# Kernel tuning notes

Hardware: AMD Instinct MI355X
Metric: run time of the kernel (lower is better)

## Reference

```python
import jax, jax.numpy as jnp
import numpy as np

K = 5          # top_k periods
KERNEL = 25    # moving-average kernel for series decomposition
D = 64         # d_model / channels
EPS = 1e-5     # BatchNorm eps (torch default)


def setup_inputs() -> dict:
    key = jax.random.key(0)
    k0, k1, k2, k3, k4 = jax.random.split(key, 5)
    B, T = 8, 2048
    x = jax.random.normal(k0, (B, T, D), jnp.float32)
    w1 = jax.random.normal(k1, (D, D, 3, 3), jnp.float32) * 0.05
    w2 = jax.random.normal(k2, (D, D, 3, 3), jnp.float32) * 0.05
    bn1_gamma = jnp.ones((D,), jnp.float32) + 0.1 * jax.random.normal(k3, (D,), jnp.float32)
    bn2_gamma = jnp.ones((D,), jnp.float32) + 0.1 * jax.random.normal(k4, (D,), jnp.float32)
    z = jnp.zeros((D,), jnp.float32)
    o = jnp.ones((D,), jnp.float32)
    return dict(x=x, w1=w1, w2=w2,
                bn1_gamma=bn1_gamma, bn1_beta=z, bn1_mean=z, bn1_var=o,
                bn2_gamma=bn2_gamma, bn2_beta=z, bn2_mean=z, bn2_var=o)


def _moving_avg(x, kernel):
    # AvgPool1d(stride=1, padding=(kernel-1)//2, count_include_pad=False) over time.
    T = x.shape[1]
    pad = (kernel - 1) // 2
    cs = jnp.concatenate([jnp.zeros_like(x[:, :1]), jnp.cumsum(x, axis=1)], axis=1)  # [B,T+1,C]
    t = jnp.arange(T)
    lo = jnp.clip(t - pad, 0, T)          # inclusive window start
    hi = jnp.clip(t + pad + 1, 0, T)      # exclusive window end
    sums = cs[:, hi] - cs[:, lo]
    return sums / (hi - lo).astype(x.dtype)[None, :, None]


def _auto_corr(s, k):
    T = s.shape[1]
    Xf = jnp.fft.rfft(s, axis=1)
    Pm = (Xf * jnp.conj(Xf)).real.mean(axis=-1)          # [B, T//2+1]
    r = jnp.fft.irfft(Pm, n=T, axis=1)                   # [B, T]
    r = r.at[:, 0].set(-jnp.inf)                          # forbid lag 0
    vals, idx = jax.lax.top_k(r, k)                       # [B,k]
    w = jax.nn.softmax(vals, axis=1)
    return idx, w


def _bn(z, gamma, beta, mean, var):
    return (z - mean) * (gamma * jax.lax.rsqrt(var + EPS)) + beta


def _process_one(s_b, p, w1, w2, bn1, bn2):
    # s_b: [T, C]; p: scalar int period.
    # Equivalent to: roll(s_b, -p), reflect-pad time to cyc*p, fold to [C,cyc,p],
    # Conv2dResBlock (3x3 zero-pad convs + eval BN + GELU + residual), unfold, crop to T.
    T, C = s_b.shape
    U = 2 * T - 2                               # static bound: cyc*p <= T+p-1 <= 2T-2
    u = jnp.arange(U)
    cyc = (T + p - 1) // p
    v = jnp.where(u < T, u, 2 * T - 2 - u)      # reflect extension index
    g = s_b[(v + p) % T]                         # [U,C] rolled-by-(-p) then reflect-padded
    r = u // p                                   # grid row (cycle)
    c = u % p                                    # grid col (phase)

    def conv3x3(z, w):
        # zero-padded 3x3 conv on the [cyc, p] grid, expressed on the flat time axis
        out = jnp.zeros_like(z)
        for dr in (-1, 0, 1):
            for dc in (-1, 0, 1):
                valid = (r + dr >= 0) & (r + dr < cyc) & (c + dc >= 0) & (c + dc < p)
                un = jnp.clip(u + dr * p + dc, 0, U - 1)
                zn = jnp.where(valid[:, None], z[un], 0.0)    # [U,C]
                out = out + zn @ w[:, :, dr + 1, dc + 1].T    # [U,Cout]
        return out

    h = _bn(conv3x3(g, w1), *bn1)
    h = jax.nn.gelu(h, approximate=False)
    h = _bn(conv3x3(h, w2), *bn2)
    return (g + h)[:T]                           # residual + unfold-crop


def reference(x, w1, w2, bn1_gamma, bn1_beta, bn1_mean, bn1_var,
              bn2_gamma, bn2_beta, bn2_mean, bn2_var):
    trend = _moving_avg(x, KERNEL)
    s = x - trend                                # seasonal
    idx, w = _auto_corr(s, K)                    # [B,K] periods, weights
    bn1 = (bn1_gamma, bn1_beta, bn1_mean, bn1_var)
    bn2 = (bn2_gamma, bn2_beta, bn2_mean, bn2_var)
    f = lambda sb, p: _process_one(sb, p, w1, w2, bn1, bn2)
    y = jax.vmap(lambda sb, pb: jax.vmap(lambda p: f(sb, p))(pb))(s, idx)  # [B,K,T,C]
    agg = jnp.einsum('bk,bktc->btc', w, y)
    return agg + trend + x
```

## Files before the change

### kernel.cpp

```cpp
#include <hip/hip_runtime.h>
#include <hip/hip_bf16.h>
#include <math.h>

#define TB 8
#define TT 2048
#define TD 64
#define TK 5
#define TPAD 12
#define EPSBN 1e-5f
#define UMAX 4096

#define ROWS 64
#define BAND 66
#define LROWS 198

#define ROWS2 32
#define BAND2 34
#define LROWS2 102
#define SH8   816
#define BUFB  13056

typedef __attribute__((ext_vector_type(8))) short short8;
typedef __attribute__((ext_vector_type(4))) float f32x4;

#define OFF_S     0
#define OFF_SBF   1048576
#define OFF_R     1572864
#define OFF_IDX   1581056
#define OFF_W     1581096
#define OFF_WT1   1581136
#define OFF_WT2   1599568
#define OFF_H1    1618000

__global__ __launch_bounds__(256) void k_trend(const float* __restrict__ x,
                                               float* __restrict__ out, float* __restrict__ s,
                                               __hip_bfloat16* __restrict__ sbf,
                                               const float* __restrict__ w1, const float* __restrict__ w2,
                                               __hip_bfloat16* __restrict__ wt1, __hip_bfloat16* __restrict__ wt2)
{
    if (blockIdx.x >= 256) {
        int d = (blockIdx.x - 256) * 256 + threadIdx.x;
        if (d < 36864) {
            int j = d & 7, l = (d >> 3) & 63, nt = (d >> 9) & 3, kb = d >> 11;
            int tap = kb >> 1, half = kb & 1;
            int co = nt * 16 + (l & 15);
            int ci = half * 32 + (l >> 4) * 8 + j;
            int src = (co * 64 + ci) * 9 + tap;
            wt1[d] = __float2bfloat16(w1[src]);
            wt2[d] = __float2bfloat16(w2[src]);
        }
        return;
    }
    int gid = blockIdx.x * 256 + threadIdx.x;
    int c = gid & 63;
    int tblk = (gid >> 6) & 127;
    int b = gid >> 13;
    int t0 = tblk * 16;
    const float* base = x + (size_t)b * TT * TD + c;
    float sum = 0.f;
    for (int tt = t0 - TPAD; tt <= t0 + TPAD; ++tt)
        if (tt >= 0 && tt < TT) sum += base[(size_t)tt * TD];
    size_t o = (size_t)b * TT * TD + (size_t)t0 * TD + c;
    #pragma unroll
    for (int i = 0; i < 16; ++i) {
        int t = t0 + i;
        int lo = t - TPAD; if (lo < 0) lo = 0;
        int hi = t + TPAD; if (hi > TT - 1) hi = TT - 1;
        float tr = sum / (float)(hi - lo + 1);
        float xv = base[(size_t)t * TD];
        out[o] = xv + tr;
        float sv = xv - tr;
        s[o] = sv;
        sbf[o] = __float2bfloat16(sv);
        int addt = t + TPAD + 1, subt = t - TPAD;
        if (addt < TT) sum += base[(size_t)addt * TD];
        if (subt >= 0) sum -= base[(size_t)subt * TD];
        o += TD;
    }
}

__global__ __launch_bounds__(256) void k_autocorr(const float* __restrict__ s, float* __restrict__ r)
{
    int b = blockIdx.z;
    int l0 = blockIdx.x * 16 + 1;
    const float* sb = s + (size_t)b * TT * TD;
    int cg = (threadIdx.x & 15) * 4;
    int tg = threadIdx.x >> 4;
    int t0 = blockIdx.y * 1024 + tg * 64;
    const int RB = TD * 4;
    const int TTB = TT * TD * 4;
    float acc[16];
    #pragma unroll
    for (int j = 0; j < 16; ++j) acc[j] = 0.f;
    float4 win[16];
    int wi = t0 + l0; if (wi >= TT) wi -= TT;
    int woff = wi * RB + cg * 4;
    int aoff = t0 * RB + cg * 4;
    #pragma unroll
    for (int m = 0; m < 16; ++m) {
        win[m] = *(const float4*)((const char*)sb + woff);
        woff += RB; if (woff >= TTB) woff -= TTB;
    }
    for (int it = 0; it < 4; ++it) {
        #pragma unroll
        for (int jj = 0; jj < 16; ++jj) {
            float4 a = *(const float4*)((const char*)sb + aoff);
            aoff += RB;
            #pragma unroll
            for (int j = 0; j < 16; ++j) {
                float4 w = win[(jj + j) & 15];
                acc[j] = fmaf(a.x, w.x, acc[j]);
                acc[j] = fmaf(a.y, w.y, acc[j]);
                acc[j] = fmaf(a.z, w.z, acc[j]);
                acc[j] = fmaf(a.w, w.w, acc[j]);
            }
            win[jj] = *(const float4*)((const char*)sb + woff);
            woff += RB; if (woff >= TTB) woff -= TTB;
        }
    }
    __shared__ float red[16 * 256];
    #pragma unroll
    for (int j = 0; j < 16; ++j) red[j * 256 + threadIdx.x] = acc[j];
    __syncthreads();
    int j = threadIdx.x >> 4, i = threadIdx.x & 15;
    float v = 0.f;
    #pragma unroll
    for (int m = 0; m < 16; ++m) v += red[j * 256 + i + 16 * m];
    #pragma unroll
    for (int mask = 8; mask; mask >>= 1) v += __shfl_xor(v, mask);
    if (i == 0) atomicAdd(&r[(size_t)b * 1024 + (l0 - 1 + j)], v * (1.0f / 64.0f));
}

__global__ __launch_bounds__(256) void k_topk(const float* __restrict__ r,
                                              int* __restrict__ selidx, float* __restrict__ selw)
{
    int b = blockIdx.x;
    __shared__ float v[1024];
    __shared__ float redv[256]; __shared__ int redi[256];
    __shared__ int s_idx[6]; __shared__ float s_val[6]; __shared__ int slots;
    for (int i = threadIdx.x; i < 1024; i += 256) v[i] = r[(size_t)b * 1024 + i];
    if (threadIdx.x == 0) slots = 0;
    __syncthreads();
    for (int round = 0; round < 5; ++round) {
        if (slots >= 5) break;
        float bv = -INFINITY; int bi = 1 << 30;
        for (int i = threadIdx.x; i < 1024; i += 256) {
            float val = v[i];
            if (val > bv) { bv = val; bi = i; }
        }
        redv[threadIdx.x] = bv; redi[threadIdx.x] = bi;
        __syncthreads();
        for (int off = 128; off; off >>= 1) {
            if (threadIdx.x < off) {
                float ov = redv[threadIdx.x + off]; int oi = redi[threadIdx.x + off];
                float mv = redv[threadIdx.x];       int mi = redi[threadIdx.x];
                if (ov > mv || (ov == mv && oi < mi)) { redv[threadIdx.x] = ov; redi[threadIdx.x] = oi; }
            }
            __syncthreads();
        }
        if (threadIdx.x == 0) {
            int lag = redi[0] + 1; float val = redv[0];
            s_idx[slots] = lag; s_val[slots] = val; slots++;
            if (slots < 5 && lag < 1024) { s_idx[slots] = 2048 - lag; s_val[slots] = val; slots++; }
            v[lag - 1] = -INFINITY;
        }
        __syncthreads();
    }
    if (threadIdx.x == 0) {
        float mx = -INFINITY;
        for (int i = 0; i < 5; ++i) mx = fmaxf(mx, s_val[i]);
        float e[5], sum = 0.f;
        for (int i = 0; i < 5; ++i) { e[i] = expf(s_val[i] - mx); sum += e[i]; }
        for (int i = 0; i < 5; ++i) { selidx[b * TK + i] = s_idx[i]; selw[b * TK + i] = e[i] / sum; }
    }
}

__global__ __launch_bounds__(128) void k_mm1(
    const short* __restrict__ s_bf, const short* __restrict__ wtp,
    const float* __restrict__ g1, const float* __restrict__ b1,
    const float* __restrict__ m1, const float* __restrict__ v1,
    const int* __restrict__ sel, __hip_bfloat16* __restrict__ h1)
{
    int b = blockIdx.z, k = blockIdx.y;
    int p = sel[b * TK + k];
    int cyc = (TT + p - 1) / p;
    int U = cyc * p;
    int u0 = blockIdx.x * ROWS;
    if (u0 >= U) return;
    __shared__ short As[LROWS * 64];

    const short* sb = s_bf + (size_t)b * TT * TD;
    for (int q = threadIdx.x; q < LROWS * 8; q += 128) {
        int row = q >> 3, ch = (q & 7) * 8;
        int band = row / BAND, i = row - band * BAND;
        int w = u0 + (band - 1) * p - 1 + i;
        int wc = min(max(w, 0), 2 * TT - 2);
        int v = (wc < TT) ? wc : (2 * TT - 2 - wc);
        int sr = (v + p) & (TT - 1);
        short8 d = *(const short8*)(sb + (size_t)sr * TD + ch);
        int off = (row * 128 + ch * 2) ^ ((row & 7) << 4);
        *(short8*)((char*)As + off) = d;
    }
    __syncthreads();

    int lane = threadIdx.x & 63;
    int wv = threadIdx.x >> 6;
    int lr = lane & 15;
    int kg = lane >> 4;
    bool inU[2], topf[2], botf[2], leftf[2], rightf[2];
    int lu[2];
    #pragma unroll
    for (int rs = 0; rs < 2; ++rs) {
        lu[rs] = wv * 32 + rs * 16 + lr;
        int u = u0 + lu[rs];
        inU[rs] = (u < U);
        int r = u / p, c = u - r * p;
        topf[rs] = (r == 0); botf[rs] = (r == cyc - 1);
        leftf[rs] = (c == 0); rightf[rs] = (c == p - 1);
    }
    f32x4 acc[2][4] = {};
    short8 zero = {};
    #pragma unroll
    for (int kb = 0; kb < 18; ++kb) {
        const int tap = kb >> 1, half = kb & 1;
        const int dr = tap / 3 - 1, dc = tap % 3 - 1;
        short8 a[2];
        #pragma unroll
        for (int rs = 0; rs < 2; ++rs) {
            int ldsrow = (dr + 1) * BAND + lu[rs] + 1 + dc;
            int off = (ldsrow * 128 + half * 64 + kg * 16) ^ ((ldsrow & 7) << 4);
            a[rs] = *(const short8*)((const char*)As + off);
            bool valid = inU[rs]
                       && !(dr == -1 && topf[rs]) && !(dr == 1 && botf[rs])
                       && !(dc == -1 && leftf[rs]) && !(dc == 1 && rightf[rs]);
            if (!valid) a[rs] = zero;
        }
        #pragma unroll
        for (int nt = 0; nt < 4; ++nt) {
            short8 bq = *(const short8*)(wtp + (size_t)(kb * 4 + nt) * 512 + lane * 8);
            #pragma unroll
            for (int rs = 0; rs < 2; ++rs)
                acc[rs][nt] = __builtin_amdgcn_mfma_f32_16x16x32_bf16(a[rs], bq, acc[rs][nt], 0, 0, 0);
        }
    }
    __hip_bfloat16* ho = h1 + (size_t)(b * TK + k) * (UMAX * TD);
    #pragma unroll
    for (int nt = 0; nt < 4; ++nt) {
        int co = nt * 16 + lr;
        float scale = g1[co] * rsqrtf(v1[co] + EPSBN);
        float bias = b1[co] - m1[co] * scale;
        #pragma unroll
        for (int rs = 0; rs < 2; ++rs) {
            int ub = u0 + wv * 32 + rs * 16 + kg * 4;
            #pragma unroll
            for (int q = 0; q < 4; ++q) {
                int u = ub + q;
                if (u < U) {
                    float z = acc[rs][nt][q] * scale + bias;
                    float ge = 0.5f * z * (1.0f + erff(z * 0.70710678118654752f));
                    ho[(size_t)u * TD + co] = __float2bfloat16(ge);
                }
            }
        }
    }
}

__global__ __launch_bounds__(128) void k_mm2f(
    const short* __restrict__ h1, const short* __restrict__ wtp,
    const float* __restrict__ s,
    const float* __restrict__ g2, const float* __restrict__ b2,
    const float* __restrict__ m2, const float* __restrict__ v2,
    const int* __restrict__ sel, const float* __restrict__ selw,
    float* __restrict__ out)
{
    int b = blockIdx.y;
    int u0 = blockIdx.x * ROWS2;
    int tid = threadIdx.x;
    __shared__ short As[2 * LROWS2 * 64];

    int lane = tid & 63, wv = tid >> 6, lr = lane & 15, kg = lane >> 4;
    int lu = wv * 16 + lr;
    int u = u0 + lu;
    const float* sb = s + (size_t)b * TT * TD;

    f32x4 accT[4] = {};
    float gacc[4][4] = {};
    short8 sreg[7];
    short8 zero = {};

    {
        int p0 = sel[b * TK];
        const short* hb = h1 + (size_t)(b * TK) * (UMAX * TD);
        #pragma unroll
        for (int it = 0; it < 7; ++it) {
            int q = tid + it * 128;
            if (q < SH8) {
                int row = q >> 3, ch = (q & 7) * 8;
                int band = row / BAND2, i = row - band * BAND2;
                int w = u0 + (band - 1) * p0 - 1 + i;
                int wc = min(max(w, 0), UMAX - 1);
                sreg[it] = *(const short8*)(hb + (size_t)wc * TD + ch);
            }
        }
        #pragma unroll
        for (int it = 0; it < 7; ++it) {
            int q = tid + it * 128;
            if (q < SH8) {
                int row = q >> 3, ch = (q & 7) * 8;
                int off = (row * 128 + ch * 2) ^ ((row & 7) << 4);
                *(short8*)((char*)As + off) = sreg[it];
            }
        }
    }
    __syncthreads();

    for (int k = 0; k < TK; ++k) {
        int p = sel[b * TK + k];
        float wk = selw[b * TK + k];
        int cyc = (TT + p - 1) / p;
        if (k < TK - 1) {
            int pn = sel[b * TK + k + 1];
            const short* hb = h1 + (size_t)(b * TK + k + 1) * (UMAX * TD);
            #pragma unroll
            for (int it = 0; it < 7; ++it) {
                int q = tid + it * 128;
                if (q < SH8) {
                    int row = q >> 3, ch = (q & 7) * 8;
                    int band = row / BAND2, i = row - band * BAND2;
                    int w = u0 + (band - 1) * pn - 1 + i;
                    int wc = min(max(w, 0), UMAX - 1);
                    sreg[it] = *(const short8*)(hb + (size_t)wc * TD + ch);
                }
            }
        }
        const char* Ab = (const char*)As + (k & 1) * BUFB;
        int r = u / p, c = u - r * p;
        bool topf = (r == 0), botf = (r == cyc - 1), leftf = (c == 0), rightf = (c == p - 1);
        f32x4 accP[4] = {};
        #pragma unroll
        for (int kb = 0; kb < 18; ++kb) {
            const int tap = kb >> 1, half = kb & 1;
            const int dr = tap / 3 - 1, dc = tap % 3 - 1;
            int ldsrow = (dr + 1) * BAND2 + lu + 1 + dc;
            int off = (ldsrow * 128 + half * 64 + kg * 16) ^ ((ldsrow & 7) << 4);
            short8 a = *(const short8*)(Ab + off);
            bool valid = !(dr == -1 && topf) && !(dr == 1 && botf)
                       && !(dc == -1 && leftf) && !(dc == 1 && rightf);
            if (!valid) a = zero;
            #pragma unroll
            for (int nt = 0; nt < 4; ++nt) {
                short8 bq = *(const short8*)(wtp + (size_t)(kb * 4 + nt) * 512 + lane * 8);
                accP[nt] = __builtin_amdgcn_mfma_f32_16x16x32_bf16(a, bq, accP[nt], 0, 0, 0);
            }
        }
        #pragma unroll
        for (int nt = 0; nt < 4; ++nt)
            #pragma unroll
            for (int e = 0; e < 4; ++e) accT[nt][e] += wk * accP[nt][e];
        #pragma unroll
        for (int q = 0; q < 4; ++q) {
            int uo = u0 + wv * 16 + kg * 4 + q;
            int sr = (uo + p) & (TT - 1);
            #pragma unroll
            for (int nt = 0; nt < 4; ++nt)
                gacc[nt][q] = fmaf(wk, sb[(size_t)sr * TD + nt * 16 + lr], gacc[nt][q]);
        }
        __syncthreads();
        if (k < TK - 1) {
            char* Aw = (char*)As + ((k + 1) & 1) * BUFB;
            #pragma unroll
            for (int it = 0; it < 7; ++it) {
                int q = tid + it * 128;
                if (q < SH8) {
                    int row = q >> 3, ch = (q & 7) * 8;
                    int off = (row * 128 + ch * 2) ^ ((row & 7) << 4);
                    *(short8*)(Aw + off) = sreg[it];
                }
            }
            __syncthreads();
        }
    }

    float* ob = out + (size_t)b * TT * TD;
    #pragma unroll
    for (int nt = 0; nt < 4; ++nt) {
        int co = nt * 16 + lr;
        float scale = g2[co] * rsqrtf(v2[co] + EPSBN);
        float bias = b2[co] - m2[co] * scale;
        #pragma unroll
        for (int q = 0; q < 4; ++q) {
            int uo = u0 + wv * 16 + kg * 4 + q;
            size_t idx = (size_t)uo * TD + co;
            ob[idx] = ob[idx] + gacc[nt][q] + scale * accT[nt][q] + bias;
        }
    }
}

extern "C" void kernel_launch(void* const* d_in, const int* in_sizes, int n_in,
                              void* d_out, int out_size, void* d_ws, size_t ws_size,
                              hipStream_t stream)
{
    const float* x  = (const float*)d_in[0];
    const float* w1 = (const float*)d_in[1];
    const float* w2 = (const float*)d_in[2];
    const float* g1 = (const float*)d_in[3];
    const float* b1 = (const float*)d_in[4];
    const float* m1 = (const float*)d_in[5];
    const float* v1 = (const float*)d_in[6];
    const float* g2 = (const float*)d_in[7];
    const float* b2 = (const float*)d_in[8];
    const float* m2 = (const float*)d_in[9];
    const float* v2 = (const float*)d_in[10];

    float* ws    = (float*)d_ws;
    float* s     = ws + OFF_S;
    __hip_bfloat16* sbf = (__hip_bfloat16*)(ws + OFF_SBF);
    float* r     = ws + OFF_R;
    int*   sel   = (int*)(ws + OFF_IDX);
    float* selw  = ws + OFF_W;
    __hip_bfloat16* wt1 = (__hip_bfloat16*)(ws + OFF_WT1);
    __hip_bfloat16* wt2 = (__hip_bfloat16*)(ws + OFF_WT2);
    __hip_bfloat16* h1  = (__hip_bfloat16*)(ws + OFF_H1);
    float* out   = (float*)d_out;

    k_trend   <<<dim3(400),         dim3(256), 0, stream>>>(x, out, s, sbf, w1, w2, wt1, wt2);
    hipMemsetAsync(r, 0, (size_t)TB * 1024 * sizeof(float), stream);
    k_autocorr<<<dim3(64, 2, TB),   dim3(256), 0, stream>>>(s, r);
    k_topk    <<<dim3(TB),          dim3(256), 0, stream>>>(r, sel, selw);
    k_mm1     <<<dim3(64, TK, TB),  dim3(128), 0, stream>>>((const short*)sbf, (const short*)wt1,
                                                            g1, b1, m1, v1, sel, h1);
    k_mm2f    <<<dim3(64, TB),      dim3(128), 0, stream>>>((const short*)h1, (const short*)wt2, s,
                                                            g2, b2, m2, v2, sel, selw, out);
}
```

Before: 142.2 us.

## Spread conv MFMA work over more waves per block in both conv kernels

k_mm1 moves to 256 threads per block, with each wave computing 16 rows instead of 32, so there are more waves and fewer accumulators per wave. k_mm2f halves the row tile to 16, doubles the grid and has each of its 4 waves own one 16-channel output slice rather than all 64 channels. The aim is more parallelism and occupancy with lower register pressure. The cost is more blocks re-staging halo rows through LDS and more redundant LDS A-tile loads across waves.

```diff
diff --git a/kernel.cpp b/kernel.cpp
--- a/kernel.cpp
+++ b/kernel.cpp
@@ -14,11 +14,11 @@
 #define BAND 66
 #define LROWS 198
 
-#define ROWS2 32
-#define BAND2 34
-#define LROWS2 102
-#define SH8   816
-#define BUFB  13056
+#define ROWS2 16
+#define BAND2 18
+#define LROWS2 54
+#define SH8   432
+#define BUFB  6912
 
 typedef __attribute__((ext_vector_type(8))) short short8;
 typedef __attribute__((ext_vector_type(4))) float f32x4;
@@ -175,7 +175,7 @@
     }
 }
 
-__global__ __launch_bounds__(128) void k_mm1(
+__global__ __launch_bounds__(256) void k_mm1(
     const short* __restrict__ s_bf, const short* __restrict__ wtp,
     const float* __restrict__ g1, const float* __restrict__ b1,
     const float* __restrict__ m1, const float* __restrict__ v1,
@@ -190,7 +190,7 @@
     __shared__ short As[LROWS * 64];
 
     const short* sb = s_bf + (size_t)b * TT * TD;
-    for (int q = threadIdx.x; q < LROWS * 8; q += 128) {
+    for (int q = threadIdx.x; q < LROWS * 8; q += 256) {
         int row = q >> 3, ch = (q & 7) * 8;
         int band = row / BAND, i = row - band * BAND;
         int w = u0 + (band - 1) * p - 1 + i;
@@ -207,40 +207,29 @@
     int wv = threadIdx.x >> 6;
     int lr = lane & 15;
     int kg = lane >> 4;
-    bool inU[2], topf[2], botf[2], leftf[2], rightf[2];
-    int lu[2];
-    #pragma unroll
-    for (int rs = 0; rs < 2; ++rs) {
-        lu[rs] = wv * 32 + rs * 16 + lr;
-        int u = u0 + lu[rs];
-        inU[rs] = (u < U);
-        int r = u / p, c = u - r * p;
-        topf[rs] = (r == 0); botf[rs] = (r == cyc - 1);
-        leftf[rs] = (c == 0); rightf[rs] = (c == p - 1);
-    }
-    f32x4 acc[2][4] = {};
+    int lu = wv * 16 + lr;
+    int u = u0 + lu;
+    bool inU = (u < U);
+    int r = u / p, c = u - r * p;
+    bool topf = (r == 0), botf = (r == cyc - 1), leftf = (c == 0), rightf = (c == p - 1);
+
+    f32x4 acc[4] = {};
     short8 zero = {};
     #pragma unroll
     for (int kb = 0; kb < 18; ++kb) {
         const int tap = kb >> 1, half = kb & 1;
         const int dr = tap / 3 - 1, dc = tap % 3 - 1;
-        short8 a[2];
-        #pragma unroll
-        for (int rs = 0; rs < 2; ++rs) {
-            int ldsrow = (dr + 1) * BAND + lu[rs] + 1 + dc;
-            int off = (ldsrow * 128 + half * 64 + kg * 16) ^ ((ldsrow & 7) << 4);
-            a[rs] = *(const short8*)((const char*)As + off);
-            bool valid = inU[rs]
-                       && !(dr == -1 && topf[rs]) && !(dr == 1 && botf[rs])
-                       && !(dc == -1 && leftf[rs]) && !(dc == 1 && rightf[rs]);
-            if (!valid) a[rs] = zero;
-        }
+        int ldsrow = (dr + 1) * BAND + lu + 1 + dc;
+        int off = (ldsrow * 128 + half * 64 + kg * 16) ^ ((ldsrow & 7) << 4);
+        short8 a = *(const short8*)((const char*)As + off);
+        bool valid = inU
+                   && !(dr == -1 && topf) && !(dr == 1 && botf)
+                   && !(dc == -1 && leftf) && !(dc == 1 && rightf);
+        if (!valid) a = zero;
         #pragma unroll
         for (int nt = 0; nt < 4; ++nt) {
             short8 bq = *(const short8*)(wtp + (size_t)(kb * 4 + nt) * 512 + lane * 8);
-            #pragma unroll
-            for (int rs = 0; rs < 2; ++rs)
-                acc[rs][nt] = __builtin_amdgcn_mfma_f32_16x16x32_bf16(a[rs], bq, acc[rs][nt], 0, 0, 0);
+            acc[nt] = __builtin_amdgcn_mfma_f32_16x16x32_bf16(a, bq, acc[nt], 0, 0, 0);
         }
     }
     __hip_bfloat16* ho = h1 + (size_t)(b * TK + k) * (UMAX * TD);
@@ -250,22 +239,18 @@
         float scale = g1[co] * rsqrtf(v1[co] + EPSBN);
         float bias = b1[co] - m1[co] * scale;
         #pragma unroll
-        for (int rs = 0; rs < 2; ++rs) {
-            int ub = u0 + wv * 32 + rs * 16 + kg * 4;
-            #pragma unroll
-            for (int q = 0; q < 4; ++q) {
-                int u = ub + q;
-                if (u < U) {
-                    float z = acc[rs][nt][q] * scale + bias;
-                    float ge = 0.5f * z * (1.0f + erff(z * 0.70710678118654752f));
-                    ho[(size_t)u * TD + co] = __float2bfloat16(ge);
-                }
-            }
-        }
-    }
-}
-
-__global__ __launch_bounds__(128) void k_mm2f(
+        for (int q = 0; q < 4; ++q) {
+            int uo = u0 + wv * 16 + kg * 4 + q;
+            if (uo < U) {
+                float z = acc[nt][q] * scale + bias;
+                float ge = 0.5f * z * (1.0f + erff(z * 0.70710678118654752f));
+                ho[(size_t)uo * TD + co] = __float2bfloat16(ge);
+            }
+        }
+    }
+}
+
+__global__ __launch_bounds__(256) void k_mm2f(
     const short* __restrict__ h1, const short* __restrict__ wtp,
     const float* __restrict__ s,
     const float* __restrict__ g2, const float* __restrict__ b2,
@@ -279,36 +264,28 @@
     __shared__ short As[2 * LROWS2 * 64];
 
     int lane = tid & 63, wv = tid >> 6, lr = lane & 15, kg = lane >> 4;
-    int lu = wv * 16 + lr;
-    int u = u0 + lu;
+    int u = u0 + lr;
     const float* sb = s + (size_t)b * TT * TD;
 
-    f32x4 accT[4] = {};
-    float gacc[4][4] = {};
-    short8 sreg[7];
+    f32x4 accT = {};
+    float gacc[4] = {0.f, 0.f, 0.f, 0.f};
+    short8 sreg[2];
     short8 zero = {};
 
     {
         int p0 = sel[b * TK];
         const short* hb = h1 + (size_t)(b * TK) * (UMAX * TD);
         #pragma unroll
-        for (int it = 0; it < 7; ++it) {
-            int q = tid + it * 128;
+        for (int it = 0; it < 2; ++it) {
+            int q = tid + it * 256;
             if (q < SH8) {
                 int row = q >> 3, ch = (q & 7) * 8;
                 int band = row / BAND2, i = row - band * BAND2;
                 int w = u0 + (band - 1) * p0 - 1 + i;
                 int wc = min(max(w, 0), UMAX - 1);
-                sreg[it] = *(const short8*)(hb + (size_t)wc * TD + ch);
-            }
-        }
-        #pragma unroll
-        for (int it = 0; it < 7; ++it) {
-            int q = tid + it * 128;
-            if (q < SH8) {
-                int row = q >> 3, ch = (q & 7) * 8;
+                short8 d = *(const short8*)(hb + (size_t)wc * TD + ch);
                 int off = (row * 128 + ch * 2) ^ ((row & 7) << 4);
-                *(short8*)((char*)As + off) = sreg[it];
+                *(short8*)((char*)As + off) = d;
             }
         }
     }
@@ -322,8 +299,8 @@
             int pn = sel[b * TK + k + 1];
             const short* hb = h1 + (size_t)(b * TK + k + 1) * (UMAX * TD);
             #pragma unroll
-            for (int it = 0; it < 7; ++it) {
-                int q = tid + it * 128;
+            for (int it = 0; it < 2; ++it) {
+                int q = tid + it * 256;
                 if (q < SH8) {
                     int row = q >> 3, ch = (q & 7) * 8;
                     int band = row / BAND2, i = row - band * BAND2;
@@ -336,41 +313,34 @@
         const char* Ab = (const char*)As + (k & 1) * BUFB;
         int r = u / p, c = u - r * p;
         bool topf = (r == 0), botf = (r == cyc - 1), leftf = (c == 0), rightf = (c == p - 1);
-        f32x4 accP[4] = {};
+        f32x4 accP[2] = {};
         #pragma unroll
         for (int kb = 0; kb < 18; ++kb) {
             const int tap = kb >> 1, half = kb & 1;
             const int dr = tap / 3 - 1, dc = tap % 3 - 1;
-            int ldsrow = (dr + 1) * BAND2 + lu + 1 + dc;
+            int ldsrow = (dr + 1) * BAND2 + lr + 1 + dc;
             int off = (ldsrow * 128 + half * 64 + kg * 16) ^ ((ldsrow & 7) << 4);
             short8 a = *(const short8*)(Ab + off);
             bool valid = !(dr == -1 && topf) && !(dr == 1 && botf)
                        && !(dc == -1 && leftf) && !(dc == 1 && rightf);
             if (!valid) a = zero;
-            #pragma unroll
-            for (int nt = 0; nt < 4; ++nt) {
-                short8 bq = *(const short8*)(wtp + (size_t)(kb * 4 + nt) * 512 + lane * 8);
-                accP[nt] = __builtin_amdgcn_mfma_f32_16x16x32_bf16(a, bq, accP[nt], 0, 0, 0);
-            }
-        }
-        #pragma unroll
-        for (int nt = 0; nt < 4; ++nt)
-            #pragma unroll
-            for (int e = 0; e < 4; ++e) accT[nt][e] += wk * accP[nt][e];
+            short8 bq = *(const short8*)(wtp + (size_t)(kb * 4 + wv) * 512 + lane * 8);
+            accP[kb & 1] = __builtin_amdgcn_mfma_f32_16x16x32_bf16(a, bq, accP[kb & 1], 0, 0, 0);
+        }
+        #pragma unroll
+        for (int e = 0; e < 4; ++e) accT[e] += wk * (accP[0][e] + accP[1][e]);
         #pragma unroll
         for (int q = 0; q < 4; ++q) {
-            int uo = u0 + wv * 16 + kg * 4 + q;
+            int uo = u0 + kg * 4 + q;
             int sr = (uo + p) & (TT - 1);
-            #pragma unroll
-            for (int nt = 0; nt < 4; ++nt)
-                gacc[nt][q] = fmaf(wk, sb[(size_t)sr * TD + nt * 16 + lr], gacc[nt][q]);
+            gacc[q] = fmaf(wk, sb[(size_t)sr * TD + wv * 16 + lr], gacc[q]);
         }
         __syncthreads();
         if (k < TK - 1) {
             char* Aw = (char*)As + ((k + 1) & 1) * BUFB;
             #pragma unroll
-            for (int it = 0; it < 7; ++it) {
-                int q = tid + it * 128;
+            for (int it = 0; it < 2; ++it) {
+                int q = tid + it * 256;
                 if (q < SH8) {
                     int row = q >> 3, ch = (q & 7) * 8;
                     int off = (row * 128 + ch * 2) ^ ((row & 7) << 4);
@@ -382,17 +352,14 @@
     }
 
     float* ob = out + (size_t)b * TT * TD;
-    #pragma unroll
-    for (int nt = 0; nt < 4; ++nt) {
-        int co = nt * 16 + lr;
-        float scale = g2[co] * rsqrtf(v2[co] + EPSBN);
-        float bias = b2[co] - m2[co] * scale;
-        #pragma unroll
-        for (int q = 0; q < 4; ++q) {
-            int uo = u0 + wv * 16 + kg * 4 + q;
-            size_t idx = (size_t)uo * TD + co;
-            ob[idx] = ob[idx] + gacc[nt][q] + scale * accT[nt][q] + bias;
-        }
+    int co = wv * 16 + lr;
+    float scale = g2[co] * rsqrtf(v2[co] + EPSBN);
+    float bias = b2[co] - m2[co] * scale;
+    #pragma unroll
+    for (int q = 0; q < 4; ++q) {
+        int uo = u0 + kg * 4 + q;
+        size_t idx = (size_t)uo * TD + co;
+        ob[idx] = ob[idx] + gacc[q] + scale * accT[q] + bias;
     }
 }
 
@@ -427,8 +394,8 @@
     hipMemsetAsync(r, 0, (size_t)TB * 1024 * sizeof(float), stream);
     k_autocorr<<<dim3(64, 2, TB),   dim3(256), 0, stream>>>(s, r);
     k_topk    <<<dim3(TB),          dim3(256), 0, stream>>>(r, sel, selw);
-    k_mm1     <<<dim3(64, TK, TB),  dim3(128), 0, stream>>>((const short*)sbf, (const short*)wt1,
+    k_mm1     <<<dim3(64, TK, TB),  dim3(256), 0, stream>>>((const short*)sbf, (const short*)wt1,
                                                             g1, b1, m1, v1, sel, h1);
-    k_mm2f    <<<dim3(64, TB),      dim3(128), 0, stream>>>((const short*)h1, (const short*)wt2, s,
+    k_mm2f    <<<dim3(128, TB),     dim3(256), 0, stream>>>((const short*)h1, (const short*)wt2, s,
                                                             g2, b2, m2, v2, sel, selw, out);
 }
```

New measurement: 121.8 us. -14.4%, faster.
